# Optimization experiments

Hardware: AMD Instinct MI355X
Metric: run time of the kernel (lower is better)

## Reference

```python
import jax, jax.numpy as jnp
import numpy as np

N = 10000      # nodes
E = 160000     # edges (before self loops)
F_IN = 78      # atom features
C = 128        # output_dim per head
H = 10         # heads in gat1
G = 64         # graphs in batch


def gat_conv(x, src, dst, n_nodes, W, a_src, a_dst, heads, ch):
    # x: [N, Fin]; W: [Fin, heads*ch]; a_src/a_dst: [heads, ch]
    h = (x @ W).reshape(-1, heads, ch)                      # [N, H, C]
    alpha_src = (h * a_src).sum(-1)                         # [N, H]
    alpha_dst = (h * a_dst).sum(-1)                         # [N, H]
    e = jax.nn.leaky_relu(alpha_src[src] + alpha_dst[dst], 0.2)  # [E, H]
    # segment softmax over edges grouped by destination node
    m = jax.ops.segment_max(e, dst, num_segments=n_nodes)
    m = jnp.where(jnp.isfinite(m), m, 0.0)
    ex = jnp.exp(e - m[dst])
    den = jax.ops.segment_sum(ex, dst, num_segments=n_nodes)
    alpha = ex / (den[dst] + 1e-16)                         # [E, H]
    out = jax.ops.segment_sum(h[src] * alpha[:, :, None], dst,
                              num_segments=n_nodes)          # [N, H, C]
    return out, alpha


def setup_inputs() -> dict:
    key = jax.random.key(0)
    ks = jax.random.split(key, 12)
    x = jax.random.normal(ks[0], (N, F_IN), dtype=jnp.float32)
    edge_index = jax.random.randint(ks[1], (2, E), 0, N, dtype=jnp.int64)
    batch = jnp.sort(jax.random.randint(ks[2], (N,), 0, G, dtype=jnp.int64))
    s1 = 1.0 / np.sqrt(F_IN)
    s2 = 1.0 / np.sqrt(H * C)
    W1 = jax.random.normal(ks[3], (F_IN, H * C), jnp.float32) * s1
    att_src1 = jax.random.normal(ks[4], (H, C), jnp.float32) * 0.1
    att_dst1 = jax.random.normal(ks[5], (H, C), jnp.float32) * 0.1
    b1 = jnp.zeros((H * C,), jnp.float32)
    W2 = jax.random.normal(ks[6], (H * C, C), jnp.float32) * s2
    att_src2 = jax.random.normal(ks[7], (1, C), jnp.float32) * 0.1
    att_dst2 = jax.random.normal(ks[8], (1, C), jnp.float32) * 0.1
    b2 = jnp.zeros((C,), jnp.float32)
    return {"x": x, "edge_index": edge_index, "batch": batch,
            "W1": W1, "att_src1": att_src1, "att_dst1": att_dst1, "b1": b1,
            "W2": W2, "att_src2": att_src2, "att_dst2": att_dst2, "b2": b2}


def reference(x, edge_index, batch, W1, att_src1, att_dst1, b1,
              W2, att_src2, att_dst2, b2):
    n = x.shape[0]
    loops = jnp.arange(n, dtype=edge_index.dtype)
    src = jnp.concatenate([edge_index[0], loops])  # PyG adds self loops
    dst = jnp.concatenate([edge_index[1], loops])
    # layer 1: 10 heads, concat
    h1, alpha1 = gat_conv(x, src, dst, n, W1, att_src1, att_dst1, H, C)
    h1 = jax.nn.elu(h1.reshape(n, H * C) + b1)     # dropout skipped (eval)
    # layer 2: 1 head
    h2, _ = gat_conv(h1, src, dst, n, W2, att_src2, att_dst2, 1, C)
    h2 = jax.nn.elu(h2.reshape(n, C) + b2)
    # global max pool per graph
    pooled = jax.ops.segment_max(h2, batch, num_segments=G)  # [G, C]
    return pooled, alpha1
```

## Files before the change

### kernel.cpp

```cpp
#include <hip/hip_runtime.h>
#include <hip/hip_bf16.h>

#define FIN 78
#define CDIM 128
#define HEADS 10
#define HC 1280
#define GRAPHS 64

typedef __bf16 bf16x8 __attribute__((ext_vector_type(8)));
typedef __bf16 bf16x4 __attribute__((ext_vector_type(4)));
typedef float f32x4 __attribute__((ext_vector_type(4)));

__global__ void init_kernel(unsigned* counts, unsigned* cursor, unsigned* pooled_u,
                            float* h2p, float* as1, float* ad1, float* as2, float* ad2,
                            int N) {
    int t = blockIdx.x * 256 + threadIdx.x;
    if (t < N) { counts[t] = 0u; cursor[t] = 0u; as2[t] = 0.f; ad2[t] = 0.f; }
    if (t < GRAPHS * CDIM) pooled_u[t] = 0x007FFFFFu;
    if (t < N * CDIM) h2p[t] = 0.f;
    if (t < N * HEADS) { as1[t] = 0.f; ad1[t] = 0.f; }
}

__global__ __launch_bounds__(256) void gemm1_mfma_kernel(
        const float* __restrict__ x, const float* __restrict__ W1,
        const float* __restrict__ asrc, const float* __restrict__ adst,
        __bf16* __restrict__ h1pb, float* __restrict__ as1, float* __restrict__ ad1,
        int M) {
    __shared__ __align__(16) __bf16 Alds[64][104];
    __shared__ __align__(16) __bf16 Blds[64][104];
    const int tid = threadIdx.x;
    const int wave = tid >> 6, lane = tid & 63;
    const int wr = wave >> 1, wc = wave & 1;
    const int m0 = blockIdx.x * 64;
    const int nbase = blockIdx.y * 256;
    const int fl = lane & 15;
    const int fh = lane >> 4;

    for (int idx = tid; idx < 64 * 96; idx += 256) {
        int m = idx / 96, k = idx % 96;
        int gm = m0 + m;
        float v = (gm < M && k < FIN) ? x[(size_t)gm * FIN + k] : 0.f;
        Alds[m][k] = (__bf16)v;
    }

    float ss[2][2][4] = {};
    float sd[2][2][4] = {};

    for (int nt = 0; nt < 4; ++nt) {
        int n0 = nbase + nt * 64;
        __syncthreads();
        for (int idx = tid; idx < 96 * 64; idx += 256) {
            int k = idx / 64, n = idx % 64;
            float v = (k < FIN) ? W1[(size_t)k * HC + n0 + n] : 0.f;
            Blds[n][k] = (__bf16)v;
        }
        __syncthreads();

        f32x4 acc[2][2] = {};
        #pragma unroll
        for (int ks = 0; ks < 96; ks += 32) {
            bf16x8 a[2], b[2];
            #pragma unroll
            for (int t = 0; t < 2; ++t) {
                a[t] = *(const bf16x8*)&Alds[wr * 32 + t * 16 + fl][ks + fh * 8];
                b[t] = *(const bf16x8*)&Blds[wc * 32 + t * 16 + fl][ks + fh * 8];
            }
            #pragma unroll
            for (int i = 0; i < 2; ++i)
                #pragma unroll
                for (int j = 0; j < 2; ++j)
                    acc[i][j] = __builtin_amdgcn_mfma_f32_16x16x32_bf16(a[i], b[j], acc[i][j], 0, 0, 0);
        }
        const int gn0 = n0 + wc * 32 + fl;
        const int gn1 = gn0 + 16;
        const float a_s0 = asrc[gn0], a_s1 = asrc[gn1];
        const float a_d0 = adst[gn0], a_d1 = adst[gn1];
        const int hI = nt >> 1;
        #pragma unroll
        for (int i = 0; i < 2; ++i)
            #pragma unroll
            for (int r = 0; r < 4; ++r) {
                int gm = m0 + wr * 32 + i * 16 + fh * 4 + r;
                if (gm < M) {
                    h1pb[(size_t)gm * HC + gn0] = (__bf16)acc[i][0][r];
                    h1pb[(size_t)gm * HC + gn1] = (__bf16)acc[i][1][r];
                }
                ss[hI][i][r] += acc[i][0][r] * a_s0 + acc[i][1][r] * a_s1;
                sd[hI][i][r] += acc[i][0][r] * a_d0 + acc[i][1][r] * a_d1;
            }
    }
    #pragma unroll
    for (int hI = 0; hI < 2; ++hI)
        #pragma unroll
        for (int i = 0; i < 2; ++i)
            #pragma unroll
            for (int r = 0; r < 4; ++r) {
                float vs = ss[hI][i][r], vd = sd[hI][i][r];
                #pragma unroll
                for (int off = 1; off < 16; off <<= 1) {
                    vs += __shfl_xor(vs, off);
                    vd += __shfl_xor(vd, off);
                }
                if (fl == 0) {
                    int gm = m0 + wr * 32 + i * 16 + fh * 4 + r;
                    if (gm < M) {
                        int hh = blockIdx.y * 2 + hI;
                        atomicAdd(&as1[gm * HEADS + hh], vs);
                        atomicAdd(&ad1[gm * HEADS + hh], vd);
                    }
                }
            }
}

__global__ __launch_bounds__(256) void gemm2_mfma_kernel(
        const __bf16* __restrict__ A, const float* __restrict__ W2,
        const float* __restrict__ asrc2, const float* __restrict__ adst2,
        float* __restrict__ C, float* __restrict__ as2, float* __restrict__ ad2, int M) {
    constexpr int BK = 64;
    constexpr int KCHUNK = HC / 2;
    __shared__ __align__(16) __bf16 Alds[64][BK + 8];
    __shared__ __align__(16) __bf16 Blds[64][BK + 8];
    const int tid = threadIdx.x;
    const int wave = tid >> 6, lane = tid & 63;
    const int wr = wave >> 1, wc = wave & 1;
    const int m0 = blockIdx.x * 64;
    const int n0 = blockIdx.y * 64;
    const int kbase = blockIdx.z * KCHUNK;

    const int kslot = (tid & 7) * 8;
    const int srow  = tid >> 3;
    const int fl = lane & 15;
    const int fh = lane >> 4;

    f32x4 acc[2][2] = {};

    for (int k0 = kbase; k0 < kbase + KCHUNK; k0 += BK) {
        #pragma unroll
        for (int rp = 0; rp < 2; ++rp) {
            int r = srow + rp * 32;
            int gm = m0 + r;
            bf16x8 va = {};
            if (gm < M) va = *(const bf16x8*)(A + (size_t)gm * HC + k0 + kslot);
            *(bf16x8*)&Alds[r][kslot] = va;
        }
        for (int idx = tid; idx < 64 * 64; idx += 256) {
            int k = idx >> 6, n = idx & 63;
            Blds[n][k] = (__bf16)W2[(size_t)(k0 + k) * CDIM + n0 + n];
        }
        __syncthreads();
        #pragma unroll
        for (int ks = 0; ks < BK; ks += 32) {
            bf16x8 a[2], b[2];
            #pragma unroll
            for (int t = 0; t < 2; ++t) {
                a[t] = *(const bf16x8*)&Alds[wr * 32 + t * 16 + fl][ks + fh * 8];
                b[t] = *(const bf16x8*)&Blds[wc * 32 + t * 16 + fl][ks + fh * 8];
            }
            #pragma unroll
            for (int i = 0; i < 2; ++i)
                #pragma unroll
                for (int j = 0; j < 2; ++j)
                    acc[i][j] = __builtin_amdgcn_mfma_f32_16x16x32_bf16(a[i], b[j], acc[i][j], 0, 0, 0);
        }
        __syncthreads();
    }
    const int gn0 = n0 + wc * 32 + fl;
    const int gn1 = gn0 + 16;
    const float a_s0 = asrc2[gn0], a_s1 = asrc2[gn1];
    const float a_d0 = adst2[gn0], a_d1 = adst2[gn1];
    #pragma unroll
    for (int i = 0; i < 2; ++i)
        #pragma unroll
        for (int r = 0; r < 4; ++r) {
            int gm = m0 + wr * 32 + i * 16 + fh * 4 + r;
            if (gm < M) {
                atomicAdd(&C[(size_t)gm * CDIM + gn0], acc[i][0][r]);
                atomicAdd(&C[(size_t)gm * CDIM + gn1], acc[i][1][r]);
            }
            float vs = acc[i][0][r] * a_s0 + acc[i][1][r] * a_s1;
            float vd = acc[i][0][r] * a_d0 + acc[i][1][r] * a_d1;
            #pragma unroll
            for (int off = 1; off < 16; off <<= 1) {
                vs += __shfl_xor(vs, off);
                vd += __shfl_xor(vd, off);
            }
            if (fl == 0 && gm < M) {
                atomicAdd(&as2[gm], vs);
                atomicAdd(&ad2[gm], vd);
            }
        }
}

__global__ void hist_kernel(const int* __restrict__ ei, int E, int N, unsigned* counts) {
    int e = blockIdx.x * 256 + threadIdx.x;
    int Et = E + N;
    if (e >= Et) return;
    int d = (e < E) ? ei[E + e] : (e - E);
    atomicAdd(&counts[d], 1u);
}

__global__ void scan_kernel(const unsigned* __restrict__ counts, unsigned* __restrict__ offsets, int n) {
    __shared__ unsigned part[1024];
    int t = threadIdx.x;
    int chunk = (n + 1023) / 1024;
    int lo = t * chunk, hi = min(lo + chunk, n);
    unsigned s = 0;
    for (int i = lo; i < hi; ++i) s += counts[i];
    part[t] = s;
    __syncthreads();
    for (int d = 1; d < 1024; d <<= 1) {
        unsigned v = (t >= d) ? part[t - d] : 0u;
        __syncthreads();
        part[t] += v;
        __syncthreads();
    }
    unsigned base = (t == 0) ? 0u : part[t - 1];
    for (int i = lo; i < hi; ++i) { offsets[i] = base; base += counts[i]; }
    if (t == 1023) offsets[n] = part[1023];
}

__global__ void scatter_kernel(const int* __restrict__ ei, int E, int N,
                               const unsigned* __restrict__ offsets, unsigned* cursor,
                               int* __restrict__ csr_src, int* __restrict__ csr_eid) {
    int e = blockIdx.x * 256 + threadIdx.x;
    int Et = E + N;
    if (e >= Et) return;
    int s, d;
    if (e < E) { s = ei[e]; d = ei[E + e]; } else { s = e - E; d = e - E; }
    unsigned pos = offsets[d] + atomicAdd(&cursor[d], 1u);
    csr_src[pos] = s;
    csr_eid[pos] = e;
}

__global__ __launch_bounds__(256) void softmax1_kernel(
        const unsigned* __restrict__ offsets,
        const int* __restrict__ csr_src, const int* __restrict__ csr_eid,
        const float* __restrict__ as1, const float* __restrict__ ad1,
        float* __restrict__ alpha_out, float* __restrict__ alpha_csr, int N) {
    const int wave = threadIdx.x >> 6, lane = threadIdx.x & 63;
    const int n = blockIdx.x * 4 + wave;
    if (n >= N) return;
    const unsigned p0 = offsets[n], p1 = offsets[n + 1];
    const unsigned deg = p1 - p0;

    float adn[HEADS];
    #pragma unroll
    for (int h = 0; h < HEADS; ++h) adn[h] = ad1[n * HEADS + h];

    if (deg <= 64) {
        const bool act = lane < (int)deg;
        const unsigned p = p0 + lane;
        int s = 0, eid = 0;
        if (act) { s = csr_src[p]; eid = csr_eid[p]; }
        const float* arow = as1 + (size_t)s * HEADS;
        float e[HEADS];
        #pragma unroll
        for (int h = 0; h < HEADS; ++h) {
            float v = act ? (arow[h] + adn[h]) : -INFINITY;
            e[h] = (v >= 0.f) ? v : 0.2f * v;
        }
        float m[HEADS];
        #pragma unroll
        for (int h = 0; h < HEADS; ++h) m[h] = e[h];
        #pragma unroll
        for (int off = 32; off; off >>= 1)
            #pragma unroll
            for (int h = 0; h < HEADS; ++h) m[h] = fmaxf(m[h], __shfl_xor(m[h], off));
        float ex[HEADS], sm[HEADS];
        #pragma unroll
        for (int h = 0; h < HEADS; ++h) {
            ex[h] = act ? __expf(e[h] - m[h]) : 0.f;
            sm[h] = ex[h];
        }
        #pragma unroll
        for (int off = 32; off; off >>= 1)
            #pragma unroll
            for (int h = 0; h < HEADS; ++h) sm[h] += __shfl_xor(sm[h], off);
        if (act) {
            #pragma unroll
            for (int h = 0; h < HEADS; ++h) {
                float a = ex[h] / (sm[h] + 1e-16f);
                alpha_csr[(size_t)p * HEADS + h] = a;
                alpha_out[(size_t)eid * HEADS + h] = a;
            }
        }
    } else {
        float m[HEADS];
        #pragma unroll
        for (int h = 0; h < HEADS; ++h) m[h] = -INFINITY;
        for (unsigned p = p0 + lane; p < p1; p += 64) {
            const float* arow = as1 + (size_t)csr_src[p] * HEADS;
            #pragma unroll
            for (int h = 0; h < HEADS; ++h) {
                float v = arow[h] + adn[h];
                v = (v >= 0.f) ? v : 0.2f * v;
                m[h] = fmaxf(m[h], v);
            }
        }
        #pragma unroll
        for (int off = 32; off; off >>= 1)
            #pragma unroll
            for (int h = 0; h < HEADS; ++h) m[h] = fmaxf(m[h], __shfl_xor(m[h], off));
        float sm[HEADS];
        #pragma unroll
        for (int h = 0; h < HEADS; ++h) sm[h] = 0.f;
        for (unsigned p = p0 + lane; p < p1; p += 64) {
            const float* arow = as1 + (size_t)csr_src[p] * HEADS;
            #pragma unroll
            for (int h = 0; h < HEADS; ++h) {
                float v = arow[h] + adn[h];
                v = (v >= 0.f) ? v : 0.2f * v;
                sm[h] += __expf(v - m[h]);
            }
        }
        #pragma unroll
        for (int off = 32; off; off >>= 1)
            #pragma unroll
            for (int h = 0; h < HEADS; ++h) sm[h] += __shfl_xor(sm[h], off);
        float inv[HEADS];
        #pragma unroll
        for (int h = 0; h < HEADS; ++h) inv[h] = 1.f / (sm[h] + 1e-16f);
        for (unsigned p = p0 + lane; p < p1; p += 64) {
            const float* arow = as1 + (size_t)csr_src[p] * HEADS;
            int eid = csr_eid[p];
            #pragma unroll
            for (int h = 0; h < HEADS; ++h) {
                float v = arow[h] + adn[h];
                v = (v >= 0.f) ? v : 0.2f * v;
                float a = __expf(v - m[h]) * inv[h];
                alpha_csr[(size_t)p * HEADS + h] = a;
                alpha_out[(size_t)eid * HEADS + h] = a;
            }
        }
    }
}

__global__ __launch_bounds__(320) void agg1_kernel(
        const unsigned* __restrict__ offsets, const int* __restrict__ csr_src,
        const float* __restrict__ alpha_csr, const __bf16* __restrict__ h1pb,
        const float* __restrict__ b1, __bf16* __restrict__ h1b, int N) {
    __shared__ float a_lds[64 * HEADS];
    __shared__ int s_lds[64];
    int n = blockIdx.x;
    unsigned p0 = offsets[n], p1 = offsets[n + 1];
    int tid = threadIdx.x;
    const int col = tid * 4;
    const int hd = tid >> 5;
    float acc[4] = {0.f, 0.f, 0.f, 0.f};
    for (unsigned base = p0; base < p1; base += 64) {
        int cnt = (int)min(64u, p1 - base);
        for (int idx = tid; idx < cnt * HEADS; idx += 320)
            a_lds[idx] = alpha_csr[(size_t)base * HEADS + idx];
        for (int idx = tid; idx < cnt; idx += 320) s_lds[idx] = csr_src[base + idx];
        __syncthreads();
        for (int j = 0; j < cnt; ++j) {
            bf16x4 hv = *(const bf16x4*)(h1pb + (size_t)s_lds[j] * HC + col);
            float a = a_lds[j * HEADS + hd];
            #pragma unroll
            for (int k = 0; k < 4; ++k) acc[k] += (float)hv[k] * a;
        }
        __syncthreads();
    }
    const float4 bv = *(const float4*)(b1 + col);
    bf16x4 outv;
    float vb[4] = {bv.x, bv.y, bv.z, bv.w};
    #pragma unroll
    for (int k = 0; k < 4; ++k) {
        float v = acc[k] + vb[k];
        v = (v > 0.f) ? v : expm1f(v);
        outv[k] = (__bf16)v;
    }
    *(bf16x4*)(h1b + (size_t)n * HC + col) = outv;
}

__device__ __forceinline__ unsigned enc_f(float f) {
    unsigned b = __float_as_uint(f);
    return (b & 0x80000000u) ? ~b : (b | 0x80000000u);
}
__device__ __forceinline__ float dec_f(unsigned k) {
    return (k & 0x80000000u) ? __uint_as_float(k & 0x7FFFFFFFu) : __uint_as_float(~k);
}

__global__ __launch_bounds__(128) void agg2_kernel(
        const unsigned* __restrict__ offsets, const int* __restrict__ csr_src,
        const float* __restrict__ as2, const float* __restrict__ ad2,
        const float* __restrict__ h2p, const float* __restrict__ b2,
        const int* __restrict__ batch, unsigned* __restrict__ pooled_u, int N) {
    const int n = blockIdx.x;
    const int tid = threadIdx.x;
    const int lane = tid & 63;
    const unsigned p0 = offsets[n], p1 = offsets[n + 1];
    const int deg = (int)(p1 - p0);
    const float adn = ad2[n];
    float acc = 0.f;

    if (deg <= 64) {
        int s_reg = 0;
        float e_reg = -INFINITY;
        if (lane < deg) {
            s_reg = csr_src[p0 + lane];
            float v = as2[s_reg] + adn;
            e_reg = (v >= 0.f) ? v : 0.2f * v;
        }
        float m = e_reg;
        #pragma unroll
        for (int off = 32; off; off >>= 1) m = fmaxf(m, __shfl_xor(m, off));
        float ex = (lane < deg) ? __expf(e_reg - m) : 0.f;
        float den = ex;
        #pragma unroll
        for (int off = 32; off; off >>= 1) den += __shfl_xor(den, off);
        float inv = 1.f / (den + 1e-16f);
        for (int j = 0; j < deg; ++j) {
            int sj = __shfl(s_reg, j);
            float aj = __shfl(ex, j) * inv;
            acc += h2p[(size_t)sj * CDIM + tid] * aj;
        }
    } else {
        float m = -INFINITY;
        for (unsigned p = p0 + lane; p < p1; p += 64) {
            float v = as2[csr_src[p]] + adn;
            v = (v >= 0.f) ? v : 0.2f * v;
            m = fmaxf(m, v);
        }
        #pragma unroll
        for (int off = 32; off; off >>= 1) m = fmaxf(m, __shfl_xor(m, off));
        float den = 0.f;
        for (unsigned p = p0 + lane; p < p1; p += 64) {
            float v = as2[csr_src[p]] + adn;
            v = (v >= 0.f) ? v : 0.2f * v;
            den += __expf(v - m);
        }
        #pragma unroll
        for (int off = 32; off; off >>= 1) den += __shfl_xor(den, off);
        float inv = 1.f / (den + 1e-16f);
        for (unsigned p = p0; p < p1; ++p) {
            int sj = csr_src[p];
            float v = as2[sj] + adn;
            v = (v >= 0.f) ? v : 0.2f * v;
            float aj = __expf(v - m) * inv;
            acc += h2p[(size_t)sj * CDIM + tid] * aj;
        }
    }
    float v = acc + b2[tid];
    v = (v > 0.f) ? v : expm1f(v);
    atomicMax(&pooled_u[batch[n] * CDIM + tid], enc_f(v));
}

__global__ void pool_write_kernel(const unsigned* __restrict__ pooled_u, float* __restrict__ out) {
    int t = blockIdx.x * 256 + threadIdx.x;
    if (t < GRAPHS * CDIM) out[t] = dec_f(pooled_u[t]);
}

extern "C" void kernel_launch(void* const* d_in, const int* in_sizes, int n_in,
                              void* d_out, int out_size, void* d_ws, size_t ws_size,
                              hipStream_t stream) {
    const float* x     = (const float*)d_in[0];
    const int*   ei    = (const int*)d_in[1];
    const int*   batch = (const int*)d_in[2];
    const float* W1    = (const float*)d_in[3];
    const float* asrc1 = (const float*)d_in[4];
    const float* adst1 = (const float*)d_in[5];
    const float* b1    = (const float*)d_in[6];
    const float* W2    = (const float*)d_in[7];
    const float* asrc2 = (const float*)d_in[8];
    const float* adst2 = (const float*)d_in[9];
    const float* b2    = (const float*)d_in[10];
    float* out = (float*)d_out;

    const int N  = in_sizes[0] / FIN;
    const int E  = in_sizes[1] / 2;
    const int Et = E + N;

    char* w = (char*)d_ws;
    auto alloc = [&](size_t nbytes) {
        char* p = w;
        w += (nbytes + 255) & ~(size_t)255;
        return p;
    };
    __bf16* h1pb = (__bf16*)alloc((size_t)N * HC * 2);
    __bf16* h1b  = (__bf16*)alloc((size_t)N * HC * 2);
    float*  h2p  = (float*)alloc((size_t)N * CDIM * 4);
    float*  as1  = (float*)alloc((size_t)N * HEADS * 4);
    float*  ad1  = (float*)alloc((size_t)N * HEADS * 4);
    float*  as2  = (float*)alloc((size_t)N * 4);
    float*  ad2  = (float*)alloc((size_t)N * 4);
    float*  alpha_csr = (float*)alloc((size_t)Et * HEADS * 4);
    unsigned* counts  = (unsigned*)alloc((size_t)N * 4);
    unsigned* cursor  = (unsigned*)alloc((size_t)N * 4);
    unsigned* offsets = (unsigned*)alloc((size_t)(N + 1) * 4);
    int* csr_src = (int*)alloc((size_t)Et * 4);
    int* csr_eid = (int*)alloc((size_t)Et * 4);
    unsigned* pooled_u = (unsigned*)alloc((size_t)GRAPHS * CDIM * 4);

    float* alpha_out = out + GRAPHS * CDIM;

    init_kernel<<<(N * CDIM + 255) / 256, 256, 0, stream>>>(
        counts, cursor, pooled_u, h2p, as1, ad1, as2, ad2, N);

    gemm1_mfma_kernel<<<dim3((N + 63) / 64, 5), 256, 0, stream>>>(
        x, W1, asrc1, adst1, h1pb, as1, ad1, N);

    hist_kernel<<<(Et + 255) / 256, 256, 0, stream>>>(ei, E, N, counts);
    scan_kernel<<<1, 1024, 0, stream>>>(counts, offsets, N);
    scatter_kernel<<<(Et + 255) / 256, 256, 0, stream>>>(ei, E, N, offsets, cursor, csr_src, csr_eid);

    softmax1_kernel<<<(N + 3) / 4, 256, 0, stream>>>(
        offsets, csr_src, csr_eid, as1, ad1, alpha_out, alpha_csr, N);
    agg1_kernel<<<N, 320, 0, stream>>>(offsets, csr_src, alpha_csr, h1pb, b1, h1b, N);

    gemm2_mfma_kernel<<<dim3((N + 63) / 64, CDIM / 64, 2), 256, 0, stream>>>(
        h1b, W2, asrc2, adst2, h2p, as2, ad2, N);

    agg2_kernel<<<N, 128, 0, stream>>>(offsets, csr_src, as2, ad2, h2p, b2, batch, pooled_u, N);

    pool_write_kernel<<<(GRAPHS * CDIM + 255) / 256, 256, 0, stream>>>(pooled_u, out);
}
```

Measured before the change: 320.9 us.

## Pre-convert inputs and weights to padded transposed bf16, retile gemm1 per head

The init kernel now converts x into a padded bf16 buffer and stores W1 and W2 as transposed bf16 copies. Both GEMMs can then fill shared memory with vectorized 16-byte loads instead of strided fp32 gathers with per-element conversion. gemm1 is retiled to 128x128 blocks with one head per block, which gives one reduction and one atomic per head per row instead of looping over four N subtiles. The cost is extra conversion work inside init (run every call), more workspace, and doubled LDS use per gemm1 block, which may lower occupancy.

```diff
diff --git a/kernel.cpp b/kernel.cpp
--- a/kernel.cpp
+++ b/kernel.cpp
@@ -6,6 +6,7 @@
 #define HEADS 10
 #define HC 1280
 #define GRAPHS 64
+#define KP 96
 
 typedef __bf16 bf16x8 __attribute__((ext_vector_type(8)));
 typedef __bf16 bf16x4 __attribute__((ext_vector_type(4)));
@@ -13,107 +14,106 @@
 
 __global__ void init_kernel(unsigned* counts, unsigned* cursor, unsigned* pooled_u,
                             float* h2p, float* as1, float* ad1, float* as2, float* ad2,
-                            int N) {
+                            const float* __restrict__ x, __bf16* __restrict__ xb,
+                            const float* __restrict__ W1, __bf16* __restrict__ W1t,
+                            const float* __restrict__ W2, __bf16* __restrict__ W2t,
+                            int N, int Mpad) {
     int t = blockIdx.x * 256 + threadIdx.x;
     if (t < N) { counts[t] = 0u; cursor[t] = 0u; as2[t] = 0.f; ad2[t] = 0.f; }
     if (t < GRAPHS * CDIM) pooled_u[t] = 0x007FFFFFu;
     if (t < N * CDIM) h2p[t] = 0.f;
     if (t < N * HEADS) { as1[t] = 0.f; ad1[t] = 0.f; }
+    if (t < Mpad * KP) {
+        int m = t / KP, k = t % KP;
+        float v = (m < N && k < FIN) ? x[(size_t)m * FIN + k] : 0.f;
+        xb[t] = (__bf16)v;
+    }
+    if (t < HC * KP) {
+        int n = t / KP, k = t % KP;
+        float v = (k < FIN) ? W1[(size_t)k * HC + n] : 0.f;
+        W1t[t] = (__bf16)v;
+    }
+    if (t < CDIM * HC) {
+        int n = t / HC, k = t % HC;
+        W2t[t] = (__bf16)W2[(size_t)k * CDIM + n];
+    }
 }
 
 __global__ __launch_bounds__(256) void gemm1_mfma_kernel(
-        const float* __restrict__ x, const float* __restrict__ W1,
+        const __bf16* __restrict__ xb, const __bf16* __restrict__ W1t,
         const float* __restrict__ asrc, const float* __restrict__ adst,
         __bf16* __restrict__ h1pb, float* __restrict__ as1, float* __restrict__ ad1,
         int M) {
-    __shared__ __align__(16) __bf16 Alds[64][104];
-    __shared__ __align__(16) __bf16 Blds[64][104];
+    __shared__ __align__(16) __bf16 Alds[128][104];
+    __shared__ __align__(16) __bf16 Blds[128][104];
     const int tid = threadIdx.x;
     const int wave = tid >> 6, lane = tid & 63;
     const int wr = wave >> 1, wc = wave & 1;
-    const int m0 = blockIdx.x * 64;
-    const int nbase = blockIdx.y * 256;
+    const int m0 = blockIdx.x * 128;
+    const int head = blockIdx.y;
+    const int n0 = head * CDIM;
     const int fl = lane & 15;
     const int fh = lane >> 4;
 
-    for (int idx = tid; idx < 64 * 96; idx += 256) {
-        int m = idx / 96, k = idx % 96;
-        int gm = m0 + m;
-        float v = (gm < M && k < FIN) ? x[(size_t)gm * FIN + k] : 0.f;
-        Alds[m][k] = (__bf16)v;
-    }
-
-    float ss[2][2][4] = {};
-    float sd[2][2][4] = {};
-
-    for (int nt = 0; nt < 4; ++nt) {
-        int n0 = nbase + nt * 64;
-        __syncthreads();
-        for (int idx = tid; idx < 96 * 64; idx += 256) {
-            int k = idx / 64, n = idx % 64;
-            float v = (k < FIN) ? W1[(size_t)k * HC + n0 + n] : 0.f;
-            Blds[n][k] = (__bf16)v;
-        }
-        __syncthreads();
-
-        f32x4 acc[2][2] = {};
-        #pragma unroll
-        for (int ks = 0; ks < 96; ks += 32) {
-            bf16x8 a[2], b[2];
-            #pragma unroll
-            for (int t = 0; t < 2; ++t) {
-                a[t] = *(const bf16x8*)&Alds[wr * 32 + t * 16 + fl][ks + fh * 8];
-                b[t] = *(const bf16x8*)&Blds[wc * 32 + t * 16 + fl][ks + fh * 8];
-            }
-            #pragma unroll
-            for (int i = 0; i < 2; ++i)
-                #pragma unroll
-                for (int j = 0; j < 2; ++j)
-                    acc[i][j] = __builtin_amdgcn_mfma_f32_16x16x32_bf16(a[i], b[j], acc[i][j], 0, 0, 0);
-        }
-        const int gn0 = n0 + wc * 32 + fl;
-        const int gn1 = gn0 + 16;
-        const float a_s0 = asrc[gn0], a_s1 = asrc[gn1];
-        const float a_d0 = adst[gn0], a_d1 = adst[gn1];
-        const int hI = nt >> 1;
-        #pragma unroll
-        for (int i = 0; i < 2; ++i)
-            #pragma unroll
-            for (int r = 0; r < 4; ++r) {
-                int gm = m0 + wr * 32 + i * 16 + fh * 4 + r;
-                if (gm < M) {
-                    h1pb[(size_t)gm * HC + gn0] = (__bf16)acc[i][0][r];
-                    h1pb[(size_t)gm * HC + gn1] = (__bf16)acc[i][1][r];
-                }
-                ss[hI][i][r] += acc[i][0][r] * a_s0 + acc[i][1][r] * a_s1;
-                sd[hI][i][r] += acc[i][0][r] * a_d0 + acc[i][1][r] * a_d1;
-            }
-    }
+    for (int idx = tid; idx < 128 * 12; idx += 256) {
+        int r = idx / 12, ks = (idx % 12) * 8;
+        *(bf16x8*)&Alds[r][ks] = *(const bf16x8*)(xb + (size_t)(m0 + r) * KP + ks);
+        *(bf16x8*)&Blds[r][ks] = *(const bf16x8*)(W1t + (size_t)(n0 + r) * KP + ks);
+    }
+    __syncthreads();
+
+    f32x4 acc[4][4] = {};
     #pragma unroll
-    for (int hI = 0; hI < 2; ++hI)
-        #pragma unroll
-        for (int i = 0; i < 2; ++i)
-            #pragma unroll
-            for (int r = 0; r < 4; ++r) {
-                float vs = ss[hI][i][r], vd = sd[hI][i][r];
-                #pragma unroll
-                for (int off = 1; off < 16; off <<= 1) {
-                    vs += __shfl_xor(vs, off);
-                    vd += __shfl_xor(vd, off);
-                }
-                if (fl == 0) {
-                    int gm = m0 + wr * 32 + i * 16 + fh * 4 + r;
-                    if (gm < M) {
-                        int hh = blockIdx.y * 2 + hI;
-                        atomicAdd(&as1[gm * HEADS + hh], vs);
-                        atomicAdd(&ad1[gm * HEADS + hh], vd);
-                    }
-                }
-            }
+    for (int ks = 0; ks < KP; ks += 32) {
+        bf16x8 a[4], b[4];
+        #pragma unroll
+        for (int t = 0; t < 4; ++t) {
+            a[t] = *(const bf16x8*)&Alds[wr * 64 + t * 16 + fl][ks + fh * 8];
+            b[t] = *(const bf16x8*)&Blds[wc * 64 + t * 16 + fl][ks + fh * 8];
+        }
+        #pragma unroll
+        for (int i = 0; i < 4; ++i)
+            #pragma unroll
+            for (int j = 0; j < 4; ++j)
+                acc[i][j] = __builtin_amdgcn_mfma_f32_16x16x32_bf16(a[i], b[j], acc[i][j], 0, 0, 0);
+    }
+
+    float a_s[4], a_d[4];
+    #pragma unroll
+    for (int j = 0; j < 4; ++j) {
+        int gn = n0 + wc * 64 + j * 16 + fl;
+        a_s[j] = asrc[gn];
+        a_d[j] = adst[gn];
+    }
+    #pragma unroll
+    for (int i = 0; i < 4; ++i) {
+        #pragma unroll
+        for (int r = 0; r < 4; ++r) {
+            int gm = m0 + wr * 64 + i * 16 + fh * 4 + r;
+            bool ok = gm < M;
+            float vs = 0.f, vd = 0.f;
+            #pragma unroll
+            for (int j = 0; j < 4; ++j) {
+                float v = acc[i][j][r];
+                if (ok) h1pb[(size_t)gm * HC + n0 + wc * 64 + j * 16 + fl] = (__bf16)v;
+                vs += v * a_s[j];
+                vd += v * a_d[j];
+            }
+            #pragma unroll
+            for (int off = 1; off < 16; off <<= 1) {
+                vs += __shfl_xor(vs, off);
+                vd += __shfl_xor(vd, off);
+            }
+            if (fl == 0 && ok) {
+                atomicAdd(&as1[gm * HEADS + head], vs);
+                atomicAdd(&ad1[gm * HEADS + head], vd);
+            }
+        }
+    }
 }
 
 __global__ __launch_bounds__(256) void gemm2_mfma_kernel(
-        const __bf16* __restrict__ A, const float* __restrict__ W2,
+        const __bf16* __restrict__ A, const __bf16* __restrict__ W2t,
         const float* __restrict__ asrc2, const float* __restrict__ adst2,
         float* __restrict__ C, float* __restrict__ as2, float* __restrict__ ad2, int M) {
     constexpr int BK = 64;
@@ -142,10 +142,7 @@
             bf16x8 va = {};
             if (gm < M) va = *(const bf16x8*)(A + (size_t)gm * HC + k0 + kslot);
             *(bf16x8*)&Alds[r][kslot] = va;
-        }
-        for (int idx = tid; idx < 64 * 64; idx += 256) {
-            int k = idx >> 6, n = idx & 63;
-            Blds[n][k] = (__bf16)W2[(size_t)(k0 + k) * CDIM + n0 + n];
+            *(bf16x8*)&Blds[r][kslot] = *(const bf16x8*)(W2t + (size_t)(n0 + r) * HC + k0 + kslot);
         }
         __syncthreads();
         #pragma unroll
@@ -470,6 +467,7 @@
     const int N  = in_sizes[0] / FIN;
     const int E  = in_sizes[1] / 2;
     const int Et = E + N;
+    const int Mpad = ((N + 127) / 128) * 128;
 
     char* w = (char*)d_ws;
     auto alloc = [&](size_t nbytes) {
@@ -479,6 +477,9 @@
     };
     __bf16* h1pb = (__bf16*)alloc((size_t)N * HC * 2);
     __bf16* h1b  = (__bf16*)alloc((size_t)N * HC * 2);
+    __bf16* xb   = (__bf16*)alloc((size_t)Mpad * KP * 2);
+    __bf16* W1t  = (__bf16*)alloc((size_t)HC * KP * 2);
+    __bf16* W2t  = (__bf16*)alloc((size_t)CDIM * HC * 2);
     float*  h2p  = (float*)alloc((size_t)N * CDIM * 4);
     float*  as1  = (float*)alloc((size_t)N * HEADS * 4);
     float*  ad1  = (float*)alloc((size_t)N * HEADS * 4);
@@ -495,10 +496,11 @@
     float* alpha_out = out + GRAPHS * CDIM;
 
     init_kernel<<<(N * CDIM + 255) / 256, 256, 0, stream>>>(
-        counts, cursor, pooled_u, h2p, as1, ad1, as2, ad2, N);
-
-    gemm1_mfma_kernel<<<dim3((N + 63) / 64, 5), 256, 0, stream>>>(
-        x, W1, asrc1, adst1, h1pb, as1, ad1, N);
+        counts, cursor, pooled_u, h2p, as1, ad1, as2, ad2,
+        x, xb, W1, W1t, W2, W2t, N, Mpad);
+
+    gemm1_mfma_kernel<<<dim3(Mpad / 128, HEADS), 256, 0, stream>>>(
+        xb, W1t, asrc1, adst1, h1pb, as1, ad1, N);
 
     hist_kernel<<<(Et + 255) / 256, 256, 0, stream>>>(ei, E, N, counts);
     scan_kernel<<<1, 1024, 0, stream>>>(counts, offsets, N);
@@ -509,7 +511,7 @@
     agg1_kernel<<<N, 320, 0, stream>>>(offsets, csr_src, alpha_csr, h1pb, b1, h1b, N);
 
     gemm2_mfma_kernel<<<dim3((N + 63) / 64, CDIM / 64, 2), 256, 0, stream>>>(
-        h1b, W2, asrc2, adst2, h2p, as2, ad2, N);
+        h1b, W2t, asrc2, adst2, h2p, as2, ad2, N);
 
     agg2_kernel<<<N, 128, 0, stream>>>(offsets, csr_src, as2, ad2, h2p, b2, batch, pooled_u, N);
 
```

Measured after the change: 277.9 us. 1.15x faster.
